# Performance work log

Hardware: AMD Instinct MI355X
Metric: run time of the kernel (lower is better)

## Reference

```python
import jax, jax.numpy as jnp
import numpy as np

VX = 1.0 / 3.2
VY = 1.0 / 3.2
X_MIN, Y_MIN = -40.0, -20.0
NX, NY = 256, 256  # grid: (40-(-40))/VX, (60-(-20))/VY
X_OFF = VX / 2.0 + X_MIN
Y_OFF = VY / 2.0 + Y_MIN


def setup_inputs() -> dict:
    key = jax.random.key(0)
    ks = jax.random.split(key, 14)
    B = 8
    Ma, Pa, Ca = 60000, 20, 5
    Mr, Pr, Cr = 80000, 32, 3
    Da, Dr, Co = 64, 64, 32
    voxels_agent = jax.random.normal(ks[0], (Ma, Pa, Ca), jnp.float32)
    coors_agent = jnp.stack([
        jax.random.randint(ks[1], (Ma,), 0, B),
        jax.random.randint(ks[2], (Ma,), 0, NY),
        jax.random.randint(ks[3], (Ma,), 0, NX)], axis=-1).astype(jnp.int32)
    num_points_agent = jax.random.randint(ks[4], (Ma,), 1, Pa + 1).astype(jnp.int32)
    voxels_rg = jax.random.normal(ks[5], (Mr, Pr, Cr), jnp.float32)
    coors_rg = jnp.stack([
        jax.random.randint(ks[6], (Mr,), 0, B),
        jax.random.randint(ks[7], (Mr,), 0, NY),
        jax.random.randint(ks[8], (Mr,), 0, NX)], axis=-1).astype(jnp.int32)
    num_points_rg = jax.random.randint(ks[9], (Mr,), 1, Pr + 1).astype(jnp.int32)
    w_agent = 0.02 * jax.random.normal(ks[10], (Ca + 5, Da), jnp.float32)
    b_agent = jnp.zeros((Da,), jnp.float32)
    w_rg = 0.02 * jax.random.normal(ks[11], (Cr + 5, Dr), jnp.float32)
    b_rg = jnp.zeros((Dr,), jnp.float32)
    conv_w = 0.02 * jax.random.normal(ks[12], (3, 3, Da + Dr, Co), jnp.float32)
    conv_b = jnp.zeros((Co,), jnp.float32)
    return dict(voxels_agent=voxels_agent, coors_agent=coors_agent,
                num_points_agent=num_points_agent, voxels_rg=voxels_rg,
                coors_rg=coors_rg, num_points_rg=num_points_rg,
                w_agent=w_agent, b_agent=b_agent, w_rg=w_rg, b_rg=b_rg,
                conv_w=conv_w, conv_b=conv_b, batch_size=B)


def _pillar_vfe(voxels, coors, num_points, W, b):
    # voxels [M,P,C]; coors [M,3]=(batch,y,x); num_points [M]
    M, P, C = voxels.shape
    mask = (jnp.arange(P)[None, :] < num_points[:, None]).astype(voxels.dtype)[..., None]  # [M,P,1]
    npts = jnp.maximum(num_points, 1).astype(voxels.dtype)[:, None, None]
    xyz = voxels[..., :3]
    mean = jnp.sum(xyz * mask, axis=1, keepdims=True) / npts          # pillar cluster mean
    f_cluster = xyz - mean                                            # [M,P,3]
    cx = coors[:, 2].astype(voxels.dtype)[:, None]
    cy = coors[:, 1].astype(voxels.dtype)[:, None]
    f_cx = voxels[..., 0] - (cx * VX + X_OFF)                         # offset from pillar center
    f_cy = voxels[..., 1] - (cy * VY + Y_OFF)
    feats = jnp.concatenate([voxels, f_cluster,
                             jnp.stack([f_cx, f_cy], axis=-1)], axis=-1) * mask  # [M,P,C+5]
    h = jax.nn.relu(feats @ W + b)                                    # [M,P,D]
    return jnp.max(h * mask, axis=1)                                  # [M,D]


def _scatter(feats, coors, B):
    # scatter pillar features into dense BEV canvas [B,NY,NX,D]
    D = feats.shape[1]
    idx = coors[:, 0] * (NY * NX) + coors[:, 1] * NX + coors[:, 2]
    canvas = jnp.zeros((B * NY * NX, D), feats.dtype).at[idx].set(feats)
    return canvas.reshape(B, NY, NX, D)


def reference(voxels_agent, coors_agent, num_points_agent, voxels_rg, coors_rg,
              num_points_rg, w_agent, b_agent, w_rg, b_rg, conv_w, conv_b,
              batch_size):
    pa = _pillar_vfe(voxels_agent, coors_agent, num_points_agent, w_agent, b_agent)
    ca = _scatter(pa, coors_agent, batch_size)
    pr = _pillar_vfe(voxels_rg, coors_rg, num_points_rg, w_rg, b_rg)
    cr = _scatter(pr, coors_rg, batch_size)
    x = jnp.concatenate([ca, cr], axis=-1)                            # [B,NY,NX,128] NHWC
    y = jax.lax.conv_general_dilated(x, conv_w, (1, 1), 'SAME',
                                     dimension_numbers=('NHWC', 'HWIO', 'NHWC'))
    return y + conv_b                                                 # [B,NY,NX,32]
```

## Files before the change

kernel.cpp:

```cpp
#include <hip/hip_runtime.h>
#include <hip/hip_bf16.h>

#define MA 60000
#define PA 20
#define CA 5
#define MR 80000
#define PR 32
#define CR 3
#define NXg 256
#define NYg 256
#define NB 8
#define NCELL (NB * NYg * NXg)

typedef __bf16 bf16x8 __attribute__((ext_vector_type(8)));
typedef float  f32x4  __attribute__((ext_vector_type(4)));
typedef float  f4     __attribute__((ext_vector_type(4)));
typedef float  f2     __attribute__((ext_vector_type(2)));

__device__ __forceinline__ unsigned short f2bf(float f) {
    unsigned int u = __float_as_uint(f);
    u += 0x7fffu + ((u >> 16) & 1u);
    return (unsigned short)(u >> 16);
}

__global__ void __launch_bounds__(256) prep_kernel(const float* __restrict__ conv_w,
                                                   unsigned short* __restrict__ bp) {
    int i = blockIdx.x * 256 + threadIdx.x;
    int j    = i & 7;
    int lane = (i >> 3) & 63;
    int nt   = (i >> 9) & 1;
    int kk   = (i >> 10) & 3;
    int tap  = i >> 12;
    int n = nt * 16 + (lane & 15);
    int k = kk * 32 + (lane >> 4) * 8 + j;
    bp[i] = f2bf(conv_w[(tap * 128 + k) * 32 + n]);
}

template <int CIN, int CF, int PMAX, int PMAXp, int WSLOT>
__device__ __forceinline__ void vfe_wave(
    int wpid, const float* __restrict__ vox, const int* __restrict__ coors,
    const int* __restrict__ npts, const float* __restrict__ W,
    const float* __restrict__ bias, unsigned short* __restrict__ feat,
    int* __restrict__ win, int M, int which, float* __restrict__ ws)
{
    constexpr int SR    = PMAXp * CIN;
    constexpr int SR4   = SR / 4;
    constexpr int PP4   = PMAXp / 4;
    constexpr int CPP   = PMAX / 4;
    constexpr int MEANOFF = 16 * SR;
    constexpr int CITER = (16 * CPP + 63) / 64;

    int lane = threadIdx.x & 63;
    int base = wpid * 16;
    if (base >= M) return;
    int cnt = M - base; cnt = cnt > 16 ? 16 : cnt;

    f4* sq    = (f4*)ws;
    f4* mean4 = (f4*)(ws + MEANOFF);

    float wc[CF];
#pragma unroll
    for (int c = 0; c < CF; ++c) wc[c] = W[c * 64 + lane];
    float bd = bias[lane];
    f2 we2[CIN];
    we2[0] = (f2){wc[0] + wc[CIN + 0] + wc[CIN + 3], wc[0] + wc[CIN + 0] + wc[CIN + 3]};
    we2[1] = (f2){wc[1] + wc[CIN + 1] + wc[CIN + 4], wc[1] + wc[CIN + 1] + wc[CIN + 4]};
    we2[2] = (f2){wc[2] + wc[CIN + 2], wc[2] + wc[CIN + 2]};
#pragma unroll
    for (int c = 3; c < CIN; ++c) we2[c] = (f2){wc[c], wc[c]};

    {
        const f4* gv = (const f4*)vox + (size_t)base * (CPP * CIN);
        int totc = cnt * CPP;
#pragma unroll
        for (int it = 0; it < CITER; ++it) {
            int c0 = it * 64 + lane;
            if (c0 < totc) {
                int p = c0 / CPP;
                int g = c0 - p * CPP;
                int npc = npts[base + p];
                npc = npc < 1 ? 1 : (npc > PMAX ? PMAX : npc);
                if (g * 4 < npc) {
                    const f4* src = gv + c0 * CIN;
                    f4 q[CIN];
#pragma unroll
                    for (int t = 0; t < CIN; ++t) q[t] = src[t];
                    float* dst = (float*)sq + p * SR + g * 4;
#pragma unroll
                    for (int cch = 0; cch < CIN; ++cch) {
                        f4 w;
#pragma unroll
                        for (int j = 0; j < 4; ++j) {
                            int e = j * CIN + cch;
                            w[j] = q[e >> 2][e & 3];
                        }
                        *(f4*)(dst + cch * PMAXp) = w;
                    }
                }
            }
        }
    }

    if (lane < cnt) {
        int np = npts[base + lane];
        np = np < 1 ? 1 : (np > PMAX ? PMAX : np);
        int np4 = (np + 3) & ~3;
        int nblk = np4 >> 2;
        float* pb = (float*)sq + lane * SR;
        float v0[CIN];
#pragma unroll
        for (int c = 0; c < CIN; ++c) v0[c] = pb[c * PMAXp];
        for (int p = np; p < np4; ++p)
#pragma unroll
            for (int c = 0; c < CIN; ++c) pb[c * PMAXp + p] = v0[c];
        const f4* pb4 = (const f4*)pb;
        f4 ax = {0.f,0.f,0.f,0.f}, ay = {0.f,0.f,0.f,0.f}, az = {0.f,0.f,0.f,0.f};
        for (int g = 0; g < nblk; ++g) {
            ax += pb4[0 * PP4 + g];
            ay += pb4[1 * PP4 + g];
            az += pb4[2 * PP4 + g];
        }
        float kf = (float)(np4 - np);
        float sx = (ax[0] + ax[1]) + (ax[2] + ax[3]) - kf * v0[0];
        float sy = (ay[0] + ay[1]) + (ay[2] + ay[3]) - kf * v0[1];
        float sz = (az[0] + az[1]) + (az[2] + az[3]) - kf * v0[2];
        float inv = 1.0f / (float)np;
        mean4[lane] = (f4){sx * inv, sy * inv, sz * inv, 0.0f};
    }

    int np_n = npts[base];
    int cb_n = coors[base * 3 + 0];
    int cy_n = coors[base * 3 + 1];
    int cx_n = coors[base * 3 + 2];

    for (int pi = 0; pi < cnt; ++pi) {
        int np = np_n, cb = cb_n, cy = cy_n, cx = cx_n;
        int pn = pi + 1;
        if (pn < cnt) {
            np_n = npts[base + pn];
            cb_n = coors[(base + pn) * 3 + 0];
            cy_n = coors[(base + pn) * 3 + 1];
            cx_n = coors[(base + pn) * 3 + 2];
        }
        np = np < 1 ? 1 : (np > PMAX ? PMAX : np);
        int nblk = (np + 3) >> 2;

        f4 m4 = mean4[pi];
        const f4* pf4 = sq + pi * SR4;
        f2 b2 = {-1e30f, -1e30f};

        for (int g = 0; g < nblk; ++g) {
            f4 v[CIN];
#pragma unroll
            for (int c = 0; c < CIN; ++c) v[c] = pf4[c * PP4 + g];
#pragma unroll
            for (int j = 0; j < 2; ++j) {
                f2 d2 = (f2){v[0][2*j], v[0][2*j+1]} * we2[0]
                      + (f2){v[1][2*j], v[1][2*j+1]} * we2[1]
                      + (f2){v[2][2*j], v[2][2*j+1]} * we2[2];
#pragma unroll
                for (int c = 3; c < CIN; ++c)
                    d2 += (f2){v[c][2*j], v[c][2*j+1]} * we2[c];
                b2 = __builtin_elementwise_max(b2, d2);
            }
        }

        float sbest = fmaxf(b2[0], b2[1]);
        float xo = (float)cx * 0.3125f + (-39.84375f);
        float yo = (float)cy * 0.3125f + (-19.84375f);
        float off = bd - (m4[0] * wc[CIN + 0] + m4[1] * wc[CIN + 1] + m4[2] * wc[CIN + 2])
                       - xo * wc[CIN + 3] - yo * wc[CIN + 4];
        float best = fmaxf(0.0f, sbest + off);

        feat[(size_t)(base + pi) * 64 + lane] = f2bf(best);

        if (lane == 0) {
            atomicMax(&win[((cb * NYg + cy) * NXg + cx) * 2 + which], base + pi);
        }
    }
}

__global__ void __launch_bounds__(256, 6) vfe_all(
    const float* __restrict__ vox_a, const int* __restrict__ coor_a,
    const int* __restrict__ np_a, const float* __restrict__ w_a,
    const float* __restrict__ b_a, unsigned short* __restrict__ feat_a,
    const float* __restrict__ vox_r, const int* __restrict__ coor_r,
    const int* __restrict__ np_r, const float* __restrict__ w_r,
    const float* __restrict__ b_r, unsigned short* __restrict__ feat_r,
    int* __restrict__ win)
{
    constexpr int WSLOT = 1664;
    __shared__ float smem[4 * WSLOT];
    int wv = threadIdx.x >> 6;
    int w  = blockIdx.x * 4 + wv;
    int g7 = w / 7, r7 = w - g7 * 7;
    float* ws = smem + wv * WSLOT;
    if (r7 < 3)
        vfe_wave<CA, CA + 5, PA, 20, WSLOT>(g7 * 3 + r7, vox_a, coor_a, np_a,
                                            w_a, b_a, feat_a, win, MA, 0, ws);
    else
        vfe_wave<CR, CR + 5, PR, 32, WSLOT>(g7 * 4 + (r7 - 3), vox_r, coor_r, np_r,
                                            w_r, b_r, feat_r, win, MR, 1, ws);
}

__global__ void __launch_bounds__(256) conv_kernel(
    const unsigned short* __restrict__ feat_a,
    const unsigned short* __restrict__ feat_r,
    const int2* __restrict__ win2,
    const unsigned short* __restrict__ bpack,
    const float* __restrict__ conv_b,
    float* __restrict__ out)
{
    __shared__ uint4 sA[396 * 5];

    int tid  = threadIdx.x;
    int lane = tid & 63;
    int wv   = tid >> 6;
    int bid  = blockIdx.x;
    int xg = bid & 3, yg = (bid >> 2) & 63, b = bid >> 8;
    int x0 = xg * 64, y0 = yg * 4;
    int mrow = lane & 15, quad = lane >> 4;

    int wA[2] = {-1, -1}, wR[2] = {-1, -1};
#pragma unroll
    for (int r = 0; r < 2; ++r) {
        int cell = tid + r * 256;
        if (cell < 396) {
            int iy = cell / 66, ix = cell - iy * 66;
            int yy = y0 - 1 + iy, xx = x0 - 1 + ix;
            if ((unsigned)yy < 256u && (unsigned)xx < 256u) {
                int2 w2 = win2[(((b << 8) + yy) << 8) + xx];
                wA[r] = w2.x; wR[r] = w2.y;
            }
        }
    }

    f32x4 acc0[4], acc1[4];
#pragma unroll
    for (int mt = 0; mt < 4; ++mt) {
        acc0[mt] = (f32x4){0.f, 0.f, 0.f, 0.f};
        acc1[mt] = (f32x4){0.f, 0.f, 0.f, 0.f};
    }

#pragma unroll
    for (int ph = 0; ph < 4; ++ph) {
        const unsigned short* feat = (ph < 2) ? feat_a : feat_r;
        const int half = (ph & 1) * 32;

#pragma unroll
        for (int r = 0; r < 2; ++r) {
            int cell = tid + r * 256;
            if (cell < 396) {
                int w = (ph < 2) ? wA[r] : wR[r];
                uint4* dst = &sA[cell * 5];
                if (w >= 0) {
                    const uint4* src = (const uint4*)(feat + ((long)w << 6) + half);
                    dst[0] = src[0]; dst[1] = src[1];
                    dst[2] = src[2]; dst[3] = src[3];
                } else {
                    uint4 zz = {0, 0, 0, 0};
                    dst[0] = zz; dst[1] = zz; dst[2] = zz; dst[3] = zz;
                }
            }
        }
        __syncthreads();

#pragma unroll
        for (int tap = 0; tap < 9; ++tap) {
            const int dyo = tap / 3, dxo = tap % 3;
            const unsigned short* bp = bpack + tap * 4096 + ph * 1024 + lane * 8;
            bf16x8 bn0 = *(const bf16x8*)(bp);
            bf16x8 bn1 = *(const bf16x8*)(bp + 512);
            int iy = wv + dyo;
#pragma unroll
            for (int mt = 0; mt < 4; ++mt) {
                int ix = mt * 16 + mrow + dxo;
                bf16x8 a = *(const bf16x8*)(&sA[(iy * 66 + ix) * 5 + quad]);
                acc0[mt] = __builtin_amdgcn_mfma_f32_16x16x32_bf16(a, bn0, acc0[mt], 0, 0, 0);
                acc1[mt] = __builtin_amdgcn_mfma_f32_16x16x32_bf16(a, bn1, acc1[mt], 0, 0, 0);
            }
        }
        __syncthreads();
    }

    int col = lane & 15;
    float bias0 = conv_b[col];
    float bias1 = conv_b[col + 16];
    int cellbase = ((((b << 8) + y0 + wv)) << 8) + x0;
#pragma unroll
    for (int mt = 0; mt < 4; ++mt) {
#pragma unroll
        for (int r = 0; r < 4; ++r) {
            int cell = cellbase + mt * 16 + quad * 4 + r;
            float* o = out + (long)cell * 32;
            o[col]      = acc0[mt][r] + bias0;
            o[col + 16] = acc1[mt][r] + bias1;
        }
    }
}

extern "C" void kernel_launch(void* const* d_in, const int* in_sizes, int n_in,
                              void* d_out, int out_size, void* d_ws, size_t ws_size,
                              hipStream_t stream)
{
    const float* vox_a  = (const float*)d_in[0];
    const int*   coor_a = (const int*)d_in[1];
    const int*   np_a   = (const int*)d_in[2];
    const float* vox_r  = (const float*)d_in[3];
    const int*   coor_r = (const int*)d_in[4];
    const int*   np_r   = (const int*)d_in[5];
    const float* w_a    = (const float*)d_in[6];
    const float* b_a    = (const float*)d_in[7];
    const float* w_r    = (const float*)d_in[8];
    const float* b_r    = (const float*)d_in[9];
    const float* conv_w = (const float*)d_in[10];
    const float* conv_b = (const float*)d_in[11];
    float* out = (float*)d_out;

    char* ws = (char*)d_ws;
    unsigned short* feat_a = (unsigned short*)(ws);
    unsigned short* feat_r = (unsigned short*)(ws + 7680000);
    int* win               = (int*)(ws + 17920000);
    unsigned short* bpack  = (unsigned short*)(ws + 17920000 + 4194304);

    hipMemsetAsync(win, 0xFF, 2 * (size_t)NCELL * sizeof(int), stream);
    hipLaunchKernelGGL(prep_kernel, dim3(144), dim3(256), 0, stream,
                       conv_w, bpack);
    hipLaunchKernelGGL(vfe_all, dim3((3750 + 5000 + 3) / 4), dim3(256), 0, stream,
                       vox_a, coor_a, np_a, w_a, b_a, feat_a,
                       vox_r, coor_r, np_r, w_r, b_r, feat_r, win);
    hipLaunchKernelGGL(conv_kernel, dim3(2048), dim3(256), 0, stream,
                       feat_a, feat_r, (const int2*)win, bpack, conv_b, out);
}
```

Before: 198.7 us.

## Drop LDS staging in pillar VFE; stream voxel points straight from global

The VFE kernel no longer stages each wave's 16 pillars into shared memory with a transposed layout and a separate mean pass. Each wave now loops over pillars and has every lane read the same float4 voxel chunks directly from global memory (broadcast loads). It accumulates the xyz sums and the max in a single pass. Removing shared memory allows a higher occupancy hint (8 waves), at the cost of redundant per-lane global loads, serial pillar latency with no prefetch, and fully scalar rather than paired FMA math.

Result: slower. 262.1 us (+31.9%).

```diff
diff --git a/kernel.cpp b/kernel.cpp
--- a/kernel.cpp
+++ b/kernel.cpp
@@ -15,7 +15,6 @@
 typedef __bf16 bf16x8 __attribute__((ext_vector_type(8)));
 typedef float  f32x4  __attribute__((ext_vector_type(4)));
 typedef float  f4     __attribute__((ext_vector_type(4)));
-typedef float  f2     __attribute__((ext_vector_type(2)));
 
 __device__ __forceinline__ unsigned short f2bf(float f) {
     unsigned int u = __float_as_uint(f);
@@ -36,151 +35,94 @@
     bp[i] = f2bf(conv_w[(tap * 128 + k) * 32 + n]);
 }
 
-template <int CIN, int CF, int PMAX, int PMAXp, int WSLOT>
+#define EL(K) q[(K) >> 2][(K) & 3]
+
+template <int CIN, int CF, int PMAX>
 __device__ __forceinline__ void vfe_wave(
     int wpid, const float* __restrict__ vox, const int* __restrict__ coors,
     const int* __restrict__ npts, const float* __restrict__ W,
     const float* __restrict__ bias, unsigned short* __restrict__ feat,
-    int* __restrict__ win, int M, int which, float* __restrict__ ws)
-{
-    constexpr int SR    = PMAXp * CIN;
-    constexpr int SR4   = SR / 4;
-    constexpr int PP4   = PMAXp / 4;
-    constexpr int CPP   = PMAX / 4;
-    constexpr int MEANOFF = 16 * SR;
-    constexpr int CITER = (16 * CPP + 63) / 64;
+    int* __restrict__ win, int which)
+{
+    constexpr int PC4 = PMAX * CIN / 4;
 
     int lane = threadIdx.x & 63;
     int base = wpid * 16;
-    if (base >= M) return;
-    int cnt = M - base; cnt = cnt > 16 ? 16 : cnt;
-
-    f4* sq    = (f4*)ws;
-    f4* mean4 = (f4*)(ws + MEANOFF);
 
     float wc[CF];
 #pragma unroll
     for (int c = 0; c < CF; ++c) wc[c] = W[c * 64 + lane];
     float bd = bias[lane];
-    f2 we2[CIN];
-    we2[0] = (f2){wc[0] + wc[CIN + 0] + wc[CIN + 3], wc[0] + wc[CIN + 0] + wc[CIN + 3]};
-    we2[1] = (f2){wc[1] + wc[CIN + 1] + wc[CIN + 4], wc[1] + wc[CIN + 1] + wc[CIN + 4]};
-    we2[2] = (f2){wc[2] + wc[CIN + 2], wc[2] + wc[CIN + 2]};
-#pragma unroll
-    for (int c = 3; c < CIN; ++c) we2[c] = (f2){wc[c], wc[c]};
-
-    {
-        const f4* gv = (const f4*)vox + (size_t)base * (CPP * CIN);
-        int totc = cnt * CPP;
-#pragma unroll
-        for (int it = 0; it < CITER; ++it) {
-            int c0 = it * 64 + lane;
-            if (c0 < totc) {
-                int p = c0 / CPP;
-                int g = c0 - p * CPP;
-                int npc = npts[base + p];
-                npc = npc < 1 ? 1 : (npc > PMAX ? PMAX : npc);
-                if (g * 4 < npc) {
-                    const f4* src = gv + c0 * CIN;
-                    f4 q[CIN];
-#pragma unroll
-                    for (int t = 0; t < CIN; ++t) q[t] = src[t];
-                    float* dst = (float*)sq + p * SR + g * 4;
-#pragma unroll
-                    for (int cch = 0; cch < CIN; ++cch) {
-                        f4 w;
-#pragma unroll
-                        for (int j = 0; j < 4; ++j) {
-                            int e = j * CIN + cch;
-                            w[j] = q[e >> 2][e & 3];
-                        }
-                        *(f4*)(dst + cch * PMAXp) = w;
-                    }
+    float w0 = wc[0] + wc[CIN + 0] + wc[CIN + 3];
+    float w1 = wc[1] + wc[CIN + 1] + wc[CIN + 4];
+    float w2 = wc[2] + wc[CIN + 2];
+
+    for (int pi = 0; pi < 16; ++pi) {
+        int gid = base + pi;
+        int np = npts[gid];
+        np = np < 1 ? 1 : (np > PMAX ? PMAX : np);
+        int nb  = (np + 3) >> 2;
+        int rem = np - (nb - 1) * 4;
+        const f4* gp = (const f4*)vox + (size_t)gid * PC4;
+        int cb = coors[gid * 3 + 0];
+        int cy = coors[gid * 3 + 1];
+        int cx = coors[gid * 3 + 2];
+
+        float b = -1e30f, sx = 0.f, sy = 0.f, sz = 0.f;
+
+        int g = 0;
+        for (; g + 1 < nb; ++g) {
+            f4 q[CIN];
+#pragma unroll
+            for (int t = 0; t < CIN; ++t) q[t] = gp[g * CIN + t];
+#pragma unroll
+            for (int j = 0; j < 4; ++j) {
+                float x = EL(j * CIN + 0);
+                float y = EL(j * CIN + 1);
+                float z = EL(j * CIN + 2);
+                float d = x * w0 + y * w1 + z * w2;
+#pragma unroll
+                for (int c = 3; c < CIN; ++c) d += EL(j * CIN + c) * wc[c];
+                b = fmaxf(b, d);
+                sx += x; sy += y; sz += z;
+            }
+        }
+        {
+            f4 q[CIN];
+#pragma unroll
+            for (int t = 0; t < CIN; ++t) q[t] = gp[g * CIN + t];
+#pragma unroll
+            for (int j = 0; j < 4; ++j) {
+                if (j < rem) {
+                    float x = EL(j * CIN + 0);
+                    float y = EL(j * CIN + 1);
+                    float z = EL(j * CIN + 2);
+                    float d = x * w0 + y * w1 + z * w2;
+#pragma unroll
+                    for (int c = 3; c < CIN; ++c) d += EL(j * CIN + c) * wc[c];
+                    b = fmaxf(b, d);
+                    sx += x; sy += y; sz += z;
                 }
             }
         }
-    }
-
-    if (lane < cnt) {
-        int np = npts[base + lane];
-        np = np < 1 ? 1 : (np > PMAX ? PMAX : np);
-        int np4 = (np + 3) & ~3;
-        int nblk = np4 >> 2;
-        float* pb = (float*)sq + lane * SR;
-        float v0[CIN];
-#pragma unroll
-        for (int c = 0; c < CIN; ++c) v0[c] = pb[c * PMAXp];
-        for (int p = np; p < np4; ++p)
-#pragma unroll
-            for (int c = 0; c < CIN; ++c) pb[c * PMAXp + p] = v0[c];
-        const f4* pb4 = (const f4*)pb;
-        f4 ax = {0.f,0.f,0.f,0.f}, ay = {0.f,0.f,0.f,0.f}, az = {0.f,0.f,0.f,0.f};
-        for (int g = 0; g < nblk; ++g) {
-            ax += pb4[0 * PP4 + g];
-            ay += pb4[1 * PP4 + g];
-            az += pb4[2 * PP4 + g];
-        }
-        float kf = (float)(np4 - np);
-        float sx = (ax[0] + ax[1]) + (ax[2] + ax[3]) - kf * v0[0];
-        float sy = (ay[0] + ay[1]) + (ay[2] + ay[3]) - kf * v0[1];
-        float sz = (az[0] + az[1]) + (az[2] + az[3]) - kf * v0[2];
+
         float inv = 1.0f / (float)np;
-        mean4[lane] = (f4){sx * inv, sy * inv, sz * inv, 0.0f};
-    }
-
-    int np_n = npts[base];
-    int cb_n = coors[base * 3 + 0];
-    int cy_n = coors[base * 3 + 1];
-    int cx_n = coors[base * 3 + 2];
-
-    for (int pi = 0; pi < cnt; ++pi) {
-        int np = np_n, cb = cb_n, cy = cy_n, cx = cx_n;
-        int pn = pi + 1;
-        if (pn < cnt) {
-            np_n = npts[base + pn];
-            cb_n = coors[(base + pn) * 3 + 0];
-            cy_n = coors[(base + pn) * 3 + 1];
-            cx_n = coors[(base + pn) * 3 + 2];
-        }
-        np = np < 1 ? 1 : (np > PMAX ? PMAX : np);
-        int nblk = (np + 3) >> 2;
-
-        f4 m4 = mean4[pi];
-        const f4* pf4 = sq + pi * SR4;
-        f2 b2 = {-1e30f, -1e30f};
-
-        for (int g = 0; g < nblk; ++g) {
-            f4 v[CIN];
-#pragma unroll
-            for (int c = 0; c < CIN; ++c) v[c] = pf4[c * PP4 + g];
-#pragma unroll
-            for (int j = 0; j < 2; ++j) {
-                f2 d2 = (f2){v[0][2*j], v[0][2*j+1]} * we2[0]
-                      + (f2){v[1][2*j], v[1][2*j+1]} * we2[1]
-                      + (f2){v[2][2*j], v[2][2*j+1]} * we2[2];
-#pragma unroll
-                for (int c = 3; c < CIN; ++c)
-                    d2 += (f2){v[c][2*j], v[c][2*j+1]} * we2[c];
-                b2 = __builtin_elementwise_max(b2, d2);
-            }
-        }
-
-        float sbest = fmaxf(b2[0], b2[1]);
+        float mx = sx * inv, my = sy * inv, mz = sz * inv;
         float xo = (float)cx * 0.3125f + (-39.84375f);
         float yo = (float)cy * 0.3125f + (-19.84375f);
-        float off = bd - (m4[0] * wc[CIN + 0] + m4[1] * wc[CIN + 1] + m4[2] * wc[CIN + 2])
+        float off = bd - (mx * wc[CIN + 0] + my * wc[CIN + 1] + mz * wc[CIN + 2])
                        - xo * wc[CIN + 3] - yo * wc[CIN + 4];
-        float best = fmaxf(0.0f, sbest + off);
-
-        feat[(size_t)(base + pi) * 64 + lane] = f2bf(best);
+        float best = fmaxf(0.0f, b + off);
+
+        feat[(size_t)gid * 64 + lane] = f2bf(best);
 
         if (lane == 0) {
-            atomicMax(&win[((cb * NYg + cy) * NXg + cx) * 2 + which], base + pi);
-        }
-    }
-}
-
-__global__ void __launch_bounds__(256, 6) vfe_all(
+            atomicMax(&win[((cb * NYg + cy) * NXg + cx) * 2 + which], gid);
+        }
+    }
+}
+
+__global__ void __launch_bounds__(256, 8) vfe_all(
     const float* __restrict__ vox_a, const int* __restrict__ coor_a,
     const int* __restrict__ np_a, const float* __restrict__ w_a,
     const float* __restrict__ b_a, unsigned short* __restrict__ feat_a,
@@ -189,18 +131,15 @@
     const float* __restrict__ b_r, unsigned short* __restrict__ feat_r,
     int* __restrict__ win)
 {
-    constexpr int WSLOT = 1664;
-    __shared__ float smem[4 * WSLOT];
-    int wv = threadIdx.x >> 6;
-    int w  = blockIdx.x * 4 + wv;
+    int w = blockIdx.x * 4 + (threadIdx.x >> 6);
+    if (w >= 8750) return;
     int g7 = w / 7, r7 = w - g7 * 7;
-    float* ws = smem + wv * WSLOT;
     if (r7 < 3)
-        vfe_wave<CA, CA + 5, PA, 20, WSLOT>(g7 * 3 + r7, vox_a, coor_a, np_a,
-                                            w_a, b_a, feat_a, win, MA, 0, ws);
+        vfe_wave<CA, CA + 5, PA>(g7 * 3 + r7, vox_a, coor_a, np_a,
+                                 w_a, b_a, feat_a, win, 0);
     else
-        vfe_wave<CR, CR + 5, PR, 32, WSLOT>(g7 * 4 + (r7 - 3), vox_r, coor_r, np_r,
-                                            w_r, b_r, feat_r, win, MR, 1, ws);
+        vfe_wave<CR, CR + 5, PR>(g7 * 4 + (r7 - 3), vox_r, coor_r, np_r,
+                                 w_r, b_r, feat_r, win, 1);
 }
 
 __global__ void __launch_bounds__(256) conv_kernel(
@@ -326,7 +265,7 @@
     hipMemsetAsync(win, 0xFF, 2 * (size_t)NCELL * sizeof(int), stream);
     hipLaunchKernelGGL(prep_kernel, dim3(144), dim3(256), 0, stream,
                        conv_w, bpack);
-    hipLaunchKernelGGL(vfe_all, dim3((3750 + 5000 + 3) / 4), dim3(256), 0, stream,
+    hipLaunchKernelGGL(vfe_all, dim3((8750 + 3) / 4), dim3(256), 0, stream,
                        vox_a, coor_a, np_a, w_a, b_a, feat_a,
                        vox_r, coor_r, np_r, w_r, b_r, feat_r, win);
     hipLaunchKernelGGL(conv_kernel, dim3(2048), dim3(256), 0, stream,
```

## Fuse weight prep into VFE kernel and halve pillars per wave

Applied to the files above, without the earlier changes.

Folds the conv-weight bf16 packing kernel into the VFE launch as 144 extra leading blocks, which removes one kernel launch. Each wave now handles 8 pillars instead of 16, with a single 64-lane gather pass and a smaller shared-memory slot. This roughly doubles the wave count and raises occupancy, meant to hide the memory latency of the irregular gather. The cost is per-wave setup (weight loads, coordinate prefetch) paid over fewer pillars, and the code now assumes M divides evenly by 8, with the bounds check removed.

After: 184.2 us. 7.3% less time.

```diff
diff --git a/kernel.cpp b/kernel.cpp
--- a/kernel.cpp
+++ b/kernel.cpp
@@ -23,40 +23,23 @@
     return (unsigned short)(u >> 16);
 }
 
-__global__ void __launch_bounds__(256) prep_kernel(const float* __restrict__ conv_w,
-                                                   unsigned short* __restrict__ bp) {
-    int i = blockIdx.x * 256 + threadIdx.x;
-    int j    = i & 7;
-    int lane = (i >> 3) & 63;
-    int nt   = (i >> 9) & 1;
-    int kk   = (i >> 10) & 3;
-    int tap  = i >> 12;
-    int n = nt * 16 + (lane & 15);
-    int k = kk * 32 + (lane >> 4) * 8 + j;
-    bp[i] = f2bf(conv_w[(tap * 128 + k) * 32 + n]);
-}
-
-template <int CIN, int CF, int PMAX, int PMAXp, int WSLOT>
+template <int CIN, int CF, int PMAX, int PMAXp>
 __device__ __forceinline__ void vfe_wave(
     int wpid, const float* __restrict__ vox, const int* __restrict__ coors,
     const int* __restrict__ npts, const float* __restrict__ W,
     const float* __restrict__ bias, unsigned short* __restrict__ feat,
-    int* __restrict__ win, int M, int which, float* __restrict__ ws)
+    int* __restrict__ win, int which, float* __restrict__ ws)
 {
-    constexpr int SR    = PMAXp * CIN;
-    constexpr int SR4   = SR / 4;
+    constexpr int SRP   = 100;
     constexpr int PP4   = PMAXp / 4;
     constexpr int CPP   = PMAX / 4;
-    constexpr int MEANOFF = 16 * SR;
-    constexpr int CITER = (16 * CPP + 63) / 64;
+    constexpr int NCH   = 8 * CPP;
+    constexpr int MEANF = 8 * SRP;
 
     int lane = threadIdx.x & 63;
-    int base = wpid * 16;
-    if (base >= M) return;
-    int cnt = M - base; cnt = cnt > 16 ? 16 : cnt;
-
-    f4* sq    = (f4*)ws;
-    f4* mean4 = (f4*)(ws + MEANOFF);
+    int base = wpid * 8;
+
+    f4* mean4 = (f4*)(ws + MEANF);
 
     float wc[CF];
 #pragma unroll
@@ -69,44 +52,36 @@
 #pragma unroll
     for (int c = 3; c < CIN; ++c) we2[c] = (f2){wc[c], wc[c]};
 
-    {
-        const f4* gv = (const f4*)vox + (size_t)base * (CPP * CIN);
-        int totc = cnt * CPP;
-#pragma unroll
-        for (int it = 0; it < CITER; ++it) {
-            int c0 = it * 64 + lane;
-            if (c0 < totc) {
-                int p = c0 / CPP;
-                int g = c0 - p * CPP;
-                int npc = npts[base + p];
-                npc = npc < 1 ? 1 : (npc > PMAX ? PMAX : npc);
-                if (g * 4 < npc) {
-                    const f4* src = gv + c0 * CIN;
-                    f4 q[CIN];
-#pragma unroll
-                    for (int t = 0; t < CIN; ++t) q[t] = src[t];
-                    float* dst = (float*)sq + p * SR + g * 4;
-#pragma unroll
-                    for (int cch = 0; cch < CIN; ++cch) {
-                        f4 w;
-#pragma unroll
-                        for (int j = 0; j < 4; ++j) {
-                            int e = j * CIN + cch;
-                            w[j] = q[e >> 2][e & 3];
-                        }
-                        *(f4*)(dst + cch * PMAXp) = w;
-                    }
+    if (lane < NCH) {
+        int p = lane / CPP;
+        int g = lane - p * CPP;
+        int npc = npts[base + p];
+        npc = npc < 1 ? 1 : (npc > PMAX ? PMAX : npc);
+        if (g * 4 < npc) {
+            const f4* src = (const f4*)vox + ((size_t)base * CPP + lane) * CIN;
+            f4 q[CIN];
+#pragma unroll
+            for (int t = 0; t < CIN; ++t) q[t] = src[t];
+            float* dst = ws + p * SRP + g * 4;
+#pragma unroll
+            for (int cch = 0; cch < CIN; ++cch) {
+                f4 w;
+#pragma unroll
+                for (int j = 0; j < 4; ++j) {
+                    int e = j * CIN + cch;
+                    w[j] = q[e >> 2][e & 3];
                 }
-            }
-        }
-    }
-
-    if (lane < cnt) {
+                *(f4*)(dst + cch * PMAXp) = w;
+            }
+        }
+    }
+
+    if (lane < 8) {
         int np = npts[base + lane];
         np = np < 1 ? 1 : (np > PMAX ? PMAX : np);
         int np4 = (np + 3) & ~3;
         int nblk = np4 >> 2;
-        float* pb = (float*)sq + lane * SR;
+        float* pb = ws + lane * SRP;
         float v0[CIN];
 #pragma unroll
         for (int c = 0; c < CIN; ++c) v0[c] = pb[c * PMAXp];
@@ -133,10 +108,10 @@
     int cy_n = coors[base * 3 + 1];
     int cx_n = coors[base * 3 + 2];
 
-    for (int pi = 0; pi < cnt; ++pi) {
+    for (int pi = 0; pi < 8; ++pi) {
         int np = np_n, cb = cb_n, cy = cy_n, cx = cx_n;
         int pn = pi + 1;
-        if (pn < cnt) {
+        if (pn < 8) {
             np_n = npts[base + pn];
             cb_n = coors[(base + pn) * 3 + 0];
             cy_n = coors[(base + pn) * 3 + 1];
@@ -145,8 +120,8 @@
         np = np < 1 ? 1 : (np > PMAX ? PMAX : np);
         int nblk = (np + 3) >> 2;
 
+        const f4* pf4 = (const f4*)(ws + pi * SRP);
         f4 m4 = mean4[pi];
-        const f4* pf4 = sq + pi * SR4;
         f2 b2 = {-1e30f, -1e30f};
 
         for (int g = 0; g < nblk; ++g) {
@@ -187,20 +162,34 @@
     const float* __restrict__ vox_r, const int* __restrict__ coor_r,
     const int* __restrict__ np_r, const float* __restrict__ w_r,
     const float* __restrict__ b_r, unsigned short* __restrict__ feat_r,
-    int* __restrict__ win)
+    int* __restrict__ win,
+    const float* __restrict__ conv_w, unsigned short* __restrict__ bpack)
 {
-    constexpr int WSLOT = 1664;
-    __shared__ float smem[4 * WSLOT];
+    constexpr int WSLOT = 8 * 100 + 32;
+    __shared__ __align__(16) float smem[4 * WSLOT];
+    int bid = blockIdx.x;
+    if (bid < 144) {
+        int i = bid * 256 + threadIdx.x;
+        int j    = i & 7;
+        int lane = (i >> 3) & 63;
+        int nt   = (i >> 9) & 1;
+        int kk   = (i >> 10) & 3;
+        int tap  = i >> 12;
+        int n = nt * 16 + (lane & 15);
+        int k = kk * 32 + (lane >> 4) * 8 + j;
+        bpack[i] = f2bf(conv_w[(tap * 128 + k) * 32 + n]);
+        return;
+    }
     int wv = threadIdx.x >> 6;
-    int w  = blockIdx.x * 4 + wv;
+    int w  = (bid - 144) * 4 + wv;
     int g7 = w / 7, r7 = w - g7 * 7;
     float* ws = smem + wv * WSLOT;
     if (r7 < 3)
-        vfe_wave<CA, CA + 5, PA, 20, WSLOT>(g7 * 3 + r7, vox_a, coor_a, np_a,
-                                            w_a, b_a, feat_a, win, MA, 0, ws);
+        vfe_wave<CA, CA + 5, PA, 20>(g7 * 3 + r7, vox_a, coor_a, np_a,
+                                     w_a, b_a, feat_a, win, 0, ws);
     else
-        vfe_wave<CR, CR + 5, PR, 32, WSLOT>(g7 * 4 + (r7 - 3), vox_r, coor_r, np_r,
-                                            w_r, b_r, feat_r, win, MR, 1, ws);
+        vfe_wave<CR, CR + 5, PR, 32>(g7 * 4 + (r7 - 3), vox_r, coor_r, np_r,
+                                     w_r, b_r, feat_r, win, 1, ws);
 }
 
 __global__ void __launch_bounds__(256) conv_kernel(
@@ -324,11 +313,10 @@
     unsigned short* bpack  = (unsigned short*)(ws + 17920000 + 4194304);
 
     hipMemsetAsync(win, 0xFF, 2 * (size_t)NCELL * sizeof(int), stream);
-    hipLaunchKernelGGL(prep_kernel, dim3(144), dim3(256), 0, stream,
+    hipLaunchKernelGGL(vfe_all, dim3(144 + 4375), dim3(256), 0, stream,
+                       vox_a, coor_a, np_a, w_a, b_a, feat_a,
+                       vox_r, coor_r, np_r, w_r, b_r, feat_r, win,
                        conv_w, bpack);
-    hipLaunchKernelGGL(vfe_all, dim3((3750 + 5000 + 3) / 4), dim3(256), 0, stream,
-                       vox_a, coor_a, np_a, w_a, b_a, feat_a,
-                       vox_r, coor_r, np_r, w_r, b_r, feat_r, win);
     hipLaunchKernelGGL(conv_kernel, dim3(2048), dim3(256), 0, stream,
                        feat_a, feat_r, (const int2*)win, bpack, conv_b, out);
 }
```
